# Kernel optimization log

Hardware: AMD Instinct MI355X
Metric: run time of the kernel (lower is better)

Reference implementation:

```python
import jax, jax.numpy as jnp
import numpy as np

MERGE_K = 3   # merge_kernel
DS_K = 3      # ds_kernel (avg-pool kernel)
STRIDE = 2


def _unfold(x, kernel, stride):
    """Torch-style F.pad + unfold(2).unfold(3): x [N,C,H,W] -> [N,Ho,Wo,K,C],
    K = kernel**2 in row-major (dh, dw) order, padding = kernel//2 with zeros."""
    pad = kernel // 2
    N, C, H, W = x.shape
    Ho, Wo = H // stride, W // stride
    xp = jnp.pad(x, ((0, 0), (0, 0), (pad, pad), (pad, pad)))
    pats = [
        xp[:, :, di:di + stride * (Ho - 1) + 1:stride,
               dj:dj + stride * (Wo - 1) + 1:stride]
        for di in range(kernel) for dj in range(kernel)
    ]
    p = jnp.stack(pats, axis=-1)          # [N,C,Ho,Wo,K]
    return p.transpose(0, 2, 3, 4, 1)     # [N,Ho,Wo,K,C]


def setup_inputs() -> dict:
    key = jax.random.key(0)
    x = jax.random.normal(key, (32, 768, 56, 56), dtype=jnp.float32)
    return {"x": x}


def reference(x):
    # compute_kq=False: k = q = x
    # AvgPool2d(3, stride=2, padding=1), count_include_pad=True -> mean over
    # zero-padded 3x3 windows == mean over K axis of the unfold.
    q = _unfold(x, DS_K, STRIDE).mean(axis=3)   # [N,Ho,Wo,C]
    kv = _unfold(x, MERGE_K, STRIDE)            # [N,Ho,Wo,K,C]; k and v are identical unfolds of x
    scores = jnp.einsum('nhwc,nhwkc->nhwk', q, kv) / MERGE_K  # divide by merge_kernel (=3), per source
    attn = jax.nn.softmax(scores, axis=-1)      # [N,Ho,Wo,K]
    y = jnp.einsum('nhwk,nhwkc->nhwc', attn, kv)  # weighted merge
    return y.transpose(0, 3, 1, 2)              # [N,C,Ho,Wo]
```

## Files before the change

kernel.cpp:

```cpp
#include <hip/hip_runtime.h>


constexpr int N_  = 32;
constexpr int C_  = 768;
constexpr int H_  = 56;
constexpr int W_  = 56;
constexpr int HO_ = 28;
constexpr int WO_ = 28;

constexpr int SC   = 16;
constexpr int NSUB = C_ / SC;
constexpr int TW   = 58;
constexpr int TILE = SC * 3 * TW;
constexpr int HW_  = H_ * W_;

__global__ __launch_bounds__(256)
void fused_kernel(const float* __restrict__ x, float* __restrict__ out) {
    __shared__ float raw[4 + TILE + 4 + TILE];
    __shared__ float sred[8 * 252];
    __shared__ float attn_s[252];
    float* bufA = raw + 4;
    float* bufB = raw + 4 + TILE + 4;

    const int tid  = threadIdx.x;
    const int blk  = blockIdx.x;
    const int n    = blk / HO_;
    const int ho   = blk - n * HO_;
    const int row0 = 2 * ho - 1;

    for (int i = tid; i < 2 * TILE + 8; i += 256) raw[i] = 0.f;

    const float* xb = x + (size_t)n * C_ * HW_;

    auto stage = [&](float* tb, int sub) {
        const float* xs = xb + (size_t)(sub * SC) * HW_;
        for (int i = tid; i < SC * 3 * 14; i += 256) {
            int c    = i / 42;
            int rem  = i - c * 42;
            int r    = rem / 14;
            int kk   = rem - r * 14;
            int grow = row0 + r;
            if (grow >= 0) {
                float4 v = *(const float4*)(xs + (size_t)c * HW_ + (size_t)grow * W_ + 4 * kk);
                float* d = &tb[(c * 3 + r) * TW + 4 * kk];
                d[0] = v.x; d[1] = v.y; d[2] = v.z; d[3] = v.w;
            }
        }
    };

    const int g   = tid >> 5;
    const int wo  = tid & 31;
    const bool act = wo < WO_;

    float acc[9];
#pragma unroll
    for (int k = 0; k < 9; ++k) acc[k] = 0.f;

    stage(bufA, 0);
    __syncthreads();
    for (int sub = 0; sub < NSUB; ++sub) {
        float* cur = (sub & 1) ? bufB : bufA;
        float* nxt = (sub & 1) ? bufA : bufB;
        if (sub + 1 < NSUB) stage(nxt, sub + 1);
        if (act) {
#pragma unroll
            for (int cc = 0; cc < 2; ++cc) {
                const float* tp = &cur[((g * 2 + cc) * 3) * TW + 2 * wo - 1];
                float w0 = tp[0],        w1 = tp[1],          w2 = tp[2];
                float w3 = tp[TW],       w4 = tp[TW + 1],     w5 = tp[TW + 2];
                float w6 = tp[2 * TW],   w7 = tp[2 * TW + 1], w8 = tp[2 * TW + 2];
                float q = ((w0 + w1) + (w2 + w3)) + ((w4 + w5) + (w6 + w7)) + w8;
                acc[0] += q * w0; acc[1] += q * w1; acc[2] += q * w2;
                acc[3] += q * w3; acc[4] += q * w4; acc[5] += q * w5;
                acc[6] += q * w6; acc[7] += q * w7; acc[8] += q * w8;
            }
        }
        __syncthreads();
    }

    if (act) {
#pragma unroll
        for (int k = 0; k < 9; ++k) sred[g * 252 + wo * 9 + k] = acc[k];
    }
    __syncthreads();
    stage(bufA, 0);
    if (tid < 252) {
        float t = 0.f;
#pragma unroll
        for (int g2 = 0; g2 < 8; ++g2) t += sred[g2 * 252 + tid];
        attn_s[tid] = t * (1.f / 27.f);
    }
    __syncthreads();
    if (tid < WO_) {
        float* s = &attn_s[tid * 9];
        float v[9];
#pragma unroll
        for (int k = 0; k < 9; ++k) v[k] = s[k];
        float m = v[0];
#pragma unroll
        for (int k = 1; k < 9; ++k) m = fmaxf(m, v[k]);
        float d = 0.f;
#pragma unroll
        for (int k = 0; k < 9; ++k) { v[k] = __expf(v[k] - m); d += v[k]; }
        float inv = 1.f / d;
#pragma unroll
        for (int k = 0; k < 9; ++k) s[k] = v[k] * inv;
    }
    __syncthreads();

    float* op = out + (size_t)n * C_ * (HO_ * WO_) + (size_t)ho * WO_;
    for (int sub = 0; sub < NSUB; ++sub) {
        float* cur = (sub & 1) ? bufB : bufA;
        float* nxt = (sub & 1) ? bufA : bufB;
        if (sub + 1 < NSUB) stage(nxt, sub + 1);
        for (int i = tid; i < SC * WO_; i += 256) {
            int c = i / WO_;
            int w = i - c * WO_;
            const float* a  = &attn_s[w * 9];
            const float* tp = &cur[(c * 3) * TW + 2 * w - 1];
            float y = a[0] * tp[0]        + a[1] * tp[1]          + a[2] * tp[2]
                    + a[3] * tp[TW]       + a[4] * tp[TW + 1]     + a[5] * tp[TW + 2]
                    + a[6] * tp[2 * TW]   + a[7] * tp[2 * TW + 1] + a[8] * tp[2 * TW + 2];
            op[(size_t)(sub * SC + c) * (HO_ * WO_) + w] = y;
        }
        __syncthreads();
    }
}

extern "C" void kernel_launch(void* const* d_in, const int* in_sizes, int n_in,
                              void* d_out, int out_size, void* d_ws, size_t ws_size,
                              hipStream_t stream) {
    const float* x = (const float*)d_in[0];
    float* out     = (float*)d_out;
    fused_kernel<<<dim3(N_ * HO_), dim3(256), 0, stream>>>(x, out);
}
```

Before: 599.4 us.

## Stage tiles with direct global-to-LDS loads in a triple-buffered two-pass pipeline

Replaces the register-staged float4 copies into padded shared tiles with __builtin_amdgcn_global_load_lds loads into three unpadded LDS buffers. Per-thread global offsets are precomputed once, and synchronisation uses explicit vmcnt waits and raw barriers. Zero padding is now applied by multiplying edge taps with masks. The score pass and the output pass share one 96-step prefetch stream, so the output pass no longer restarts its pipeline. The goal is to hide global load latency and cut VGPR traffic and LDS store instructions. The risks are that the wo=0 tap reads just outside a buffer and relies on mask-multiplication, and that output stores counted in vmcnt may force the waits to cover the newest loads.

```diff
diff --git a/kernel.cpp b/kernel.cpp
--- a/kernel.cpp
+++ b/kernel.cpp
@@ -7,75 +7,95 @@
 constexpr int W_  = 56;
 constexpr int HO_ = 28;
 constexpr int WO_ = 28;
+constexpr int HW_ = H_ * W_;
 
-constexpr int SC   = 16;
-constexpr int NSUB = C_ / SC;
-constexpr int TW   = 58;
-constexpr int TILE = SC * 3 * TW;
-constexpr int HW_  = H_ * W_;
+constexpr int SC      = 16;
+constexpr int NSUB    = C_ / SC;
+constexpr int TILE_F4 = 768;
+
+#define WAITV3() do { asm volatile("s_waitcnt vmcnt(3)" ::: "memory"); \
+                      __builtin_amdgcn_sched_barrier(0); } while (0)
+#define WAITV0() do { asm volatile("s_waitcnt vmcnt(0)" ::: "memory"); \
+                      __builtin_amdgcn_sched_barrier(0); } while (0)
+#define RAWBAR() do { asm volatile("" ::: "memory"); __builtin_amdgcn_s_barrier(); \
+                      __builtin_amdgcn_sched_barrier(0); } while (0)
 
 __global__ __launch_bounds__(256)
 void fused_kernel(const float* __restrict__ x, float* __restrict__ out) {
-    __shared__ float raw[4 + TILE + 4 + TILE];
-    __shared__ float sred[8 * 252];
-    __shared__ float attn_s[252];
-    float* bufA = raw + 4;
-    float* bufB = raw + 4 + TILE + 4;
+    __shared__ float4 bufs[3][TILE_F4];
+    __shared__ float  sred[8 * 252];
+    __shared__ float  attn_s[252];
 
     const int tid  = threadIdx.x;
     const int blk  = blockIdx.x;
     const int n    = blk / HO_;
     const int ho   = blk - n * HO_;
     const int row0 = 2 * ho - 1;
+    const int lane = tid & 63;
+    const int wv   = tid >> 6;
 
-    for (int i = tid; i < 2 * TILE + 8; i += 256) raw[i] = 0.f;
+    int goff[3], lds4[3];
+#pragma unroll
+    for (int j = 0; j < 3; ++j) {
+        int q  = wv + 4 * j;
+        int i  = q * 64 + lane;
+        int ii = i > 671 ? 671 : i;
+        int c  = ii / 42;
+        int rem = ii - c * 42;
+        int r  = rem / 14;
+        int kk = rem - r * 14;
+        int grow = row0 + r; if (grow < 0) grow = 0;
+        goff[j] = c * HW_ + grow * W_ + 4 * kk;
+        lds4[j] = q * 64;
+    }
 
     const float* xb = x + (size_t)n * C_ * HW_;
-
-    auto stage = [&](float* tb, int sub) {
-        const float* xs = xb + (size_t)(sub * SC) * HW_;
-        for (int i = tid; i < SC * 3 * 14; i += 256) {
-            int c    = i / 42;
-            int rem  = i - c * 42;
-            int r    = rem / 14;
-            int kk   = rem - r * 14;
-            int grow = row0 + r;
-            if (grow >= 0) {
-                float4 v = *(const float4*)(xs + (size_t)c * HW_ + (size_t)grow * W_ + 4 * kk);
-                float* d = &tb[(c * 3 + r) * TW + 4 * kk];
-                d[0] = v.x; d[1] = v.y; d[2] = v.z; d[3] = v.w;
-            }
-        }
+    auto stage = [&](int sub, int bsel) {
+        const float* xs = xb + (size_t)sub * (SC * HW_);
+        float4* tb = &bufs[bsel][0];
+#pragma unroll
+        for (int j = 0; j < 3; ++j)
+            __builtin_amdgcn_global_load_lds(
+                (const __attribute__((address_space(1))) unsigned int*)(xs + goff[j]),
+                (__attribute__((address_space(3))) unsigned int*)(tb + lds4[j]),
+                16, 0, 0);
     };
 
     const int g   = tid >> 5;
     const int wo  = tid & 31;
     const bool act = wo < WO_;
+    const float mt  = (ho > 0) ? 1.f : 0.f;
+    const float ml  = (wo > 0) ? 1.f : 0.f;
+    const float mtl = mt * ml;
 
     float acc[9];
 #pragma unroll
     for (int k = 0; k < 9; ++k) acc[k] = 0.f;
 
-    stage(bufA, 0);
-    __syncthreads();
-    for (int sub = 0; sub < NSUB; ++sub) {
-        float* cur = (sub & 1) ? bufB : bufA;
-        float* nxt = (sub & 1) ? bufA : bufB;
-        if (sub + 1 < NSUB) stage(nxt, sub + 1);
+    stage(0, 0);
+    stage(1, 1);
+    WAITV3();
+    RAWBAR();
+
+    for (int t = 0; t < 48; ++t) {
+        int s = t + 2;
+        stage(s < 48 ? s : s - 48, s % 3);
+        const float* cur = (const float*)&bufs[t % 3][0];
         if (act) {
 #pragma unroll
             for (int cc = 0; cc < 2; ++cc) {
-                const float* tp = &cur[((g * 2 + cc) * 3) * TW + 2 * wo - 1];
-                float w0 = tp[0],        w1 = tp[1],          w2 = tp[2];
-                float w3 = tp[TW],       w4 = tp[TW + 1],     w5 = tp[TW + 2];
-                float w6 = tp[2 * TW],   w7 = tp[2 * TW + 1], w8 = tp[2 * TW + 2];
+                const float* tp = cur + (g * 2 + cc) * 168 + 2 * wo - 1;
+                float w0 = tp[0]   * mtl, w1 = tp[1]   * mt, w2 = tp[2]   * mt;
+                float w3 = tp[56]  * ml,  w4 = tp[57],      w5 = tp[58];
+                float w6 = tp[112] * ml,  w7 = tp[113],     w8 = tp[114];
                 float q = ((w0 + w1) + (w2 + w3)) + ((w4 + w5) + (w6 + w7)) + w8;
                 acc[0] += q * w0; acc[1] += q * w1; acc[2] += q * w2;
                 acc[3] += q * w3; acc[4] += q * w4; acc[5] += q * w5;
                 acc[6] += q * w6; acc[7] += q * w7; acc[8] += q * w8;
             }
         }
-        __syncthreads();
+        WAITV3();
+        RAWBAR();
     }
 
     if (act) {
@@ -83,7 +103,6 @@
         for (int k = 0; k < 9; ++k) sred[g * 252 + wo * 9 + k] = acc[k];
     }
     __syncthreads();
-    stage(bufA, 0);
     if (tid < 252) {
         float t = 0.f;
 #pragma unroll
@@ -108,22 +127,40 @@
     }
     __syncthreads();
 
-    float* op = out + (size_t)n * C_ * (HO_ * WO_) + (size_t)ho * WO_;
-    for (int sub = 0; sub < NSUB; ++sub) {
-        float* cur = (sub & 1) ? bufB : bufA;
-        float* nxt = (sub & 1) ? bufA : bufB;
-        if (sub + 1 < NSUB) stage(nxt, sub + 1);
-        for (int i = tid; i < SC * WO_; i += 256) {
-            int c = i / WO_;
-            int w = i - c * WO_;
-            const float* a  = &attn_s[w * 9];
-            const float* tp = &cur[(c * 3) * TW + 2 * w - 1];
-            float y = a[0] * tp[0]        + a[1] * tp[1]          + a[2] * tp[2]
-                    + a[3] * tp[TW]       + a[4] * tp[TW + 1]     + a[5] * tp[TW + 2]
-                    + a[6] * tp[2 * TW]   + a[7] * tp[2 * TW + 1] + a[8] * tp[2 * TW + 2];
-            op[(size_t)(sub * SC + c) * (HO_ * WO_) + w] = y;
+    const int cA = tid / 28, wA = tid - cA * 28;
+    const int iB = tid + 256;
+    const int cB = iB / 28, wB = iB - cB * 28;
+    const bool actB = iB < 448;
+    const float mlA = (wA > 0) ? 1.f : 0.f;
+    const float mlB = (wB > 0) ? 1.f : 0.f;
+    float* ob = out + (size_t)n * C_ * (HO_ * WO_) + (size_t)ho * WO_;
+
+    for (int t = 48; t < 96; ++t) {
+        if (t <= 93) stage(t + 2 - 48, (t + 2) % 3);
+        const float* cur = (const float*)&bufs[t % 3][0];
+        const int sub = t - 48;
+        {
+            const float* tp = cur + cA * 168 + 2 * wA - 1;
+            const float* a  = &attn_s[wA * 9];
+            float w0 = tp[0]   * (mt * mlA), w1 = tp[1]   * mt, w2 = tp[2] * mt;
+            float w3 = tp[56]  * mlA,        w4 = tp[57],       w5 = tp[58];
+            float w6 = tp[112] * mlA,        w7 = tp[113],      w8 = tp[114];
+            float y = a[0]*w0 + a[1]*w1 + a[2]*w2 + a[3]*w3 + a[4]*w4
+                    + a[5]*w5 + a[6]*w6 + a[7]*w7 + a[8]*w8;
+            ob[(size_t)(sub * SC + cA) * (HO_ * WO_) + wA] = y;
         }
-        __syncthreads();
+        if (actB) {
+            const float* tp = cur + cB * 168 + 2 * wB - 1;
+            const float* a  = &attn_s[wB * 9];
+            float w0 = tp[0]   * (mt * mlB), w1 = tp[1]   * mt, w2 = tp[2] * mt;
+            float w3 = tp[56]  * mlB,        w4 = tp[57],       w5 = tp[58];
+            float w6 = tp[112] * mlB,        w7 = tp[113],      w8 = tp[114];
+            float y = a[0]*w0 + a[1]*w1 + a[2]*w2 + a[3]*w3 + a[4]*w4
+                    + a[5]*w5 + a[6]*w6 + a[7]*w7 + a[8]*w8;
+            ob[(size_t)(sub * SC + cB) * (HO_ * WO_) + wB] = y;
+        }
+        if (t < 94) { WAITV3(); } else { WAITV0(); }
+        RAWBAR();
     }
 }
 
```

Measured after the change: 566.0 us. 5.6% less time.
